# Kernel optimization log

Hardware: AMD Instinct MI355X
Metric: run time of the kernel (lower is better)

Reference implementation:

```python
import jax, jax.numpy as jnp
import numpy as np

B, S, D = 2, 2048, 2048
H, HD = 16, 128
ROPE_BASE = 10000.0


def _rope(x):
    # x: [B, H, S, HD]; standard rotate-half RoPE with base 10000
    half = x.shape[-1] // 2
    inv_freq = 1.0 / (ROPE_BASE ** (jnp.arange(half, dtype=jnp.float32) / half))
    pos = jnp.arange(x.shape[2], dtype=jnp.float32)
    freqs = pos[:, None] * inv_freq[None, :]           # [S, half]
    cos = jnp.concatenate([jnp.cos(freqs), jnp.cos(freqs)], axis=-1)  # [S, HD]
    sin = jnp.concatenate([jnp.sin(freqs), jnp.sin(freqs)], axis=-1)
    x_rot = jnp.concatenate([-x[..., half:], x[..., :half]], axis=-1)
    return x * cos[None, None, :, :] + x_rot * sin[None, None, :, :]


def setup_inputs() -> dict:
    key = jax.random.key(0)
    kx, kq, ko = jax.random.split(key, 3)
    x = jax.random.normal(kx, (B, S, D), dtype=jnp.float32)
    # weights stored [in, out] (transposed torch Linear weight), no bias
    W_qkv = jax.random.normal(kq, (D, 3 * H * HD), dtype=jnp.float32) * (D ** -0.5)
    W_o = jax.random.normal(ko, (H * HD, D), dtype=jnp.float32) * ((H * HD) ** -0.5)
    return {"x": x, "W_qkv": W_qkv, "W_o": W_o}


def reference(x, W_qkv, W_o):
    b, s, _ = x.shape
    qkv = x @ W_qkv                                    # [B, S, 3*H*HD]
    q, k, v = jnp.split(qkv, 3, axis=-1)
    def heads(t):
        return t.reshape(b, s, H, HD).transpose(0, 2, 1, 3)  # [B, H, S, HD]
    q, k, v = heads(q), heads(k), heads(v)
    q = _rope(q)
    k = _rope(k)
    scores = jnp.einsum("bhqd,bhkd->bhqk", q, k) * (HD ** -0.5)
    causal = jnp.tril(jnp.ones((s, s), dtype=bool))
    scores = jnp.where(causal[None, None, :, :], scores, jnp.float32(-jnp.inf))
    attn = jax.nn.softmax(scores, axis=-1)
    out = jnp.einsum("bhqk,bhkd->bhqd", attn, v)       # [B, H, S, HD]
    out = out.transpose(0, 2, 1, 3).reshape(b, s, H * HD)
    return out @ W_o
```

## Files before the change

kernel.cpp:

```cpp
#include <hip/hip_runtime.h>
#include <math.h>


#define B_    2
#define S_    2048
#define D_    2048
#define H_    16
#define HD_   128
#define M_    (B_ * S_)
#define NQKV_ (3 * H_ * HD_)

typedef __bf16 bf16x8 __attribute__((ext_vector_type(8)));
typedef float  f32x4  __attribute__((ext_vector_type(4)));
typedef unsigned short u16x8 __attribute__((ext_vector_type(8)));

__device__ __forceinline__ unsigned short f32_bf16(float f) {
  unsigned int u = __float_as_uint(f);
  u = (u + 0x7fffu + ((u >> 16) & 1u)) >> 16;
  return (unsigned short)u;
}
__device__ __forceinline__ float bf16_f32(unsigned short u) {
  return __uint_as_float(((unsigned int)u) << 16);
}

__device__ __forceinline__ void gload_lds16(const void* g, void* lds) {
  __builtin_amdgcn_global_load_lds(
      (const __attribute__((address_space(1))) unsigned int*)g,
      (__attribute__((address_space(3))) unsigned int*)lds, 16, 0, 0);
}

__global__ __launch_bounds__(256) void cvt_bf16_kernel(
    const float* __restrict__ in, unsigned short* __restrict__ out, int n4) {
  int i = blockIdx.x * blockDim.x + threadIdx.x;
  if (i >= n4) return;
  float4 v = ((const float4*)in)[i];
  ((ushort4*)out)[i] =
      make_ushort4(f32_bf16(v.x), f32_bf16(v.y), f32_bf16(v.z), f32_bf16(v.w));
}

__global__ __launch_bounds__(1024) void cvt_t_kernel(
    const float* __restrict__ in, unsigned short* __restrict__ out,
    int K, int ldin, int ncol0) {
  __shared__ float t[32][33];
  const int n0 = blockIdx.x * 32, k0 = blockIdx.y * 32;
  const int tx = threadIdx.x & 31, ty = threadIdx.x >> 5;
  t[ty][tx] = in[(size_t)(k0 + ty) * ldin + ncol0 + n0 + tx];
  __syncthreads();
  out[(size_t)(n0 + ty) * K + k0 + tx] = f32_bf16(t[tx][ty]);
}

__global__ __launch_bounds__(256) void rope_bf16_kernel(
    unsigned short* __restrict__ qkv) {
  const int row = blockIdx.x;
  const int sec = blockIdx.y * 4 + (threadIdx.x >> 6);
  const int d   = threadIdx.x & 63;
  const int pos = row & (S_ - 1);
  float invf = exp2f(-(float)d * (13.287712379549449f / 64.0f));
  float ang = (float)pos * invf;
  float sn, cs;
  sincosf(ang, &sn, &cs);
  unsigned short* p = qkv + (size_t)row * NQKV_ + sec * HD_ + d;
  float x1 = bf16_f32(p[0]), x2 = bf16_f32(p[64]);
  p[0]  = f32_bf16(x1 * cs - x2 * sn);
  p[64] = f32_bf16(x2 * cs + x1 * sn);
}

template <bool OUT_BF16>
__global__ __launch_bounds__(256) void gemm_bt_bf16(
    const unsigned short* __restrict__ A, const unsigned short* __restrict__ Bt,
    void* __restrict__ Cv, int M, int N, int K, int ldc) {
  constexpr int BK = 32;
  __shared__ __align__(16) unsigned short As[128 * BK];
  __shared__ __align__(16) unsigned short Bs[128 * BK];
  const int tid = threadIdx.x;
  const int wid = tid >> 6, lane = tid & 63;
  const int wr = wid >> 1, wc = wid & 1;
  const int m0 = blockIdx.y * 128, n0 = blockIdx.x * 128;

  const char* Ab = (const char*)(A + (size_t)m0 * K);
  const char* Bb = (const char*)(Bt + (size_t)n0 * K);
  char* AsB = (char*)As;
  char* BsB = (char*)Bs;
  const size_t rowbytes = (size_t)K * 2;

  f32x4 acc[4][4];
#pragma unroll
  for (int i = 0; i < 4; ++i)
#pragma unroll
    for (int j = 0; j < 4; ++j) acc[i][j] = (f32x4){0.f, 0.f, 0.f, 0.f};

  const int r16 = lane & 15, kg = lane >> 4;

  for (int k0 = 0; k0 < K; k0 += BK) {
#pragma unroll
    for (int c = 0; c < 2; ++c) {
      int q = wid * 128 + c * 64 + lane;
      size_t goff = (size_t)(q >> 2) * rowbytes + (size_t)k0 * 2 + (q & 3) * 16;
      int loff = wid * 2048 + c * 1024;
      gload_lds16(Ab + goff, AsB + loff);
      gload_lds16(Bb + goff, BsB + loff);
    }
    __syncthreads();

    bf16x8 af[4], bfr[4];
#pragma unroll
    for (int i = 0; i < 4; ++i)
      af[i] = *(const bf16x8*)(As + (wr * 64 + i * 16 + r16) * BK + kg * 8);
#pragma unroll
    for (int j = 0; j < 4; ++j)
      bfr[j] = *(const bf16x8*)(Bs + (wc * 64 + j * 16 + r16) * BK + kg * 8);
#pragma unroll
    for (int i = 0; i < 4; ++i)
#pragma unroll
      for (int j = 0; j < 4; ++j)
        acc[i][j] = __builtin_amdgcn_mfma_f32_16x16x32_bf16(af[i], bfr[j],
                                                            acc[i][j], 0, 0, 0);
    __syncthreads();
  }

#pragma unroll
  for (int i = 0; i < 4; ++i) {
    int row = m0 + wr * 64 + i * 16 + (lane >> 4) * 4;
#pragma unroll
    for (int j = 0; j < 4; ++j) {
      int col = n0 + wc * 64 + j * 16 + (lane & 15);
      if constexpr (OUT_BF16) {
        unsigned short* cp = (unsigned short*)Cv + (size_t)row * ldc + col;
        cp[0]               = f32_bf16(acc[i][j][0]);
        cp[(size_t)ldc]     = f32_bf16(acc[i][j][1]);
        cp[(size_t)2 * ldc] = f32_bf16(acc[i][j][2]);
        cp[(size_t)3 * ldc] = f32_bf16(acc[i][j][3]);
      } else {
        float* cp = (float*)Cv + (size_t)row * ldc + col;
        cp[0]               = acc[i][j][0];
        cp[(size_t)ldc]     = acc[i][j][1];
        cp[(size_t)2 * ldc] = acc[i][j][2];
        cp[(size_t)3 * ldc] = acc[i][j][3];
      }
    }
  }
}

__global__ __launch_bounds__(256) void attn_mfma_kernel(
    const unsigned short* __restrict__ qkv, unsigned short* __restrict__ out) {
  const int qt = (int)gridDim.x - 1 - (int)blockIdx.x;
  const int bh = blockIdx.y;
  const int b = bh >> 4, h = bh & (H_ - 1);
  const int tid = threadIdx.x;
  const int w = tid >> 6, lane = tid & 63;
  const int r16 = lane & 15, kg = lane >> 4;

  __shared__ __align__(16) unsigned short Qs[64 * 128];
  __shared__ __align__(16) unsigned short Ks[64 * 128];
  __shared__ __align__(16) unsigned short Vt[128 * 72];
  __shared__ __align__(16) unsigned short Ps[4][16 * 72];

  const unsigned short* Qg = qkv + ((size_t)b * S_ + (size_t)qt * 64) * NQKV_ + h * HD_;
  const unsigned short* Kg = qkv + (size_t)b * S_ * NQKV_ + H_ * HD_ + h * HD_;
  const unsigned short* Vg = qkv + (size_t)b * S_ * NQKV_ + 2 * H_ * HD_ + h * HD_;

#pragma unroll
  for (int it = 0; it < 4; ++it) {
    int q = w * 256 + it * 64 + lane;
    int row = q >> 4, c = q & 15;
    int gc = c ^ (row & 7);
    gload_lds16(Qg + (size_t)row * NQKV_ + gc * 8, (char*)Qs + q * 16);
  }

  float m_i[4], l_i[4];
  f32x4 accO[8];
#pragma unroll
  for (int r = 0; r < 4; ++r) { m_i[r] = -INFINITY; l_i[r] = 0.f; }
#pragma unroll
  for (int jd = 0; jd < 8; ++jd) accO[jd] = (f32x4){0.f, 0.f, 0.f, 0.f};

  const float scale = 0.08838834764831845f;
  const int qg_row = qt * 64 + w * 16 + kg * 4;
  const int nkt = qt + 1;

  for (int kt = 0; kt < nkt; ++kt) {
    const int kv0 = kt * 64;
    __syncthreads();

#pragma unroll
    for (int it = 0; it < 4; ++it) {
      int q = w * 256 + it * 64 + lane;
      int row = q >> 4, c = q & 15;
      int gc = c ^ (row & 7);
      gload_lds16(Kg + (size_t)(kv0 + row) * NQKV_ + gc * 8, (char*)Ks + q * 16);
    }
    {
      const unsigned short* vr = Vg + (size_t)(kv0 + lane) * NQKV_;
#pragma unroll
      for (int it = 0; it < 4; ++it) {
        int dc = w + it * 4;
        u16x8 v = *(const u16x8*)(vr + dc * 8);
#pragma unroll
        for (int j = 0; j < 8; ++j) Vt[(dc * 8 + j) * 72 + lane] = v[j];
      }
    }
    __syncthreads();

    f32x4 sc[4];
#pragma unroll
    for (int j = 0; j < 4; ++j) sc[j] = (f32x4){0.f, 0.f, 0.f, 0.f};
    {
      const int arow = w * 16 + r16;
      bf16x8 aq[4];
#pragma unroll
      for (int ks = 0; ks < 4; ++ks)
        aq[ks] = *(const bf16x8*)((const char*)Qs + arow * 256 +
                                  (((ks * 4 + kg) ^ (arow & 7)) * 16));
#pragma unroll
      for (int ks = 0; ks < 4; ++ks) {
#pragma unroll
        for (int j = 0; j < 4; ++j) {
          const int brow = j * 16 + r16;
          bf16x8 bk = *(const bf16x8*)((const char*)Ks + brow * 256 +
                                       (((ks * 4 + kg) ^ (brow & 7)) * 16));
          sc[j] = __builtin_amdgcn_mfma_f32_16x16x32_bf16(aq[ks], bk, sc[j], 0, 0, 0);
        }
      }
    }

    const bool diag = (kt == qt);
    float alpha[4];
#pragma unroll
    for (int r = 0; r < 4; ++r) {
      float sv[4];
#pragma unroll
      for (int j = 0; j < 4; ++j) {
        sv[j] = sc[j][r] * scale;
        if (diag && (kv0 + j * 16 + r16 > qg_row + r)) sv[j] = -INFINITY;
      }
      float tmax = fmaxf(fmaxf(sv[0], sv[1]), fmaxf(sv[2], sv[3]));
#pragma unroll
      for (int off = 8; off > 0; off >>= 1)
        tmax = fmaxf(tmax, __shfl_xor(tmax, off, 16));
      float mn = fmaxf(m_i[r], tmax);
      alpha[r] = __expf(m_i[r] - mn);
      m_i[r] = mn;
      float rs = 0.f;
#pragma unroll
      for (int j = 0; j < 4; ++j) {
        float p = __expf(sv[j] - mn);
        rs += p;
        Ps[w][(kg * 4 + r) * 72 + j * 16 + r16] = f32_bf16(p);
      }
#pragma unroll
      for (int off = 8; off > 0; off >>= 1) rs += __shfl_xor(rs, off, 16);
      l_i[r] = l_i[r] * alpha[r] + rs;
    }

#pragma unroll
    for (int jd = 0; jd < 8; ++jd)
#pragma unroll
      for (int r = 0; r < 4; ++r) accO[jd][r] *= alpha[r];

#pragma unroll
    for (int ks2 = 0; ks2 < 2; ++ks2) {
      bf16x8 pf = *(const bf16x8*)((const char*)&Ps[w][0] + r16 * 144 +
                                   ks2 * 64 + kg * 16);
#pragma unroll
      for (int jd = 0; jd < 8; ++jd) {
        bf16x8 vf = *(const bf16x8*)((const char*)Vt + (jd * 16 + r16) * 144 +
                                     ks2 * 64 + kg * 16);
        accO[jd] = __builtin_amdgcn_mfma_f32_16x16x32_bf16(pf, vf, accO[jd], 0, 0, 0);
      }
    }
  }

  unsigned short* ob = out + ((size_t)b * S_ + (size_t)qt * 64 + w * 16) * (H_ * HD_) +
                       h * HD_;
#pragma unroll
  for (int r = 0; r < 4; ++r) {
    float inv_l = 1.0f / l_i[r];
    unsigned short* orow = ob + (size_t)(kg * 4 + r) * (H_ * HD_);
#pragma unroll
    for (int jd = 0; jd < 8; ++jd)
      orow[jd * 16 + r16] = f32_bf16(accO[jd][r] * inv_l);
  }
}

extern "C" void kernel_launch(void* const* d_in, const int* in_sizes, int n_in,
                              void* d_out, int out_size, void* d_ws, size_t ws_size,
                              hipStream_t stream) {
  const float* x    = (const float*)d_in[0];
  const float* Wqkv = (const float*)d_in[1];
  const float* Wo   = (const float*)d_in[2];
  float* out = (float*)d_out;

  char* ws = (char*)d_ws;
  unsigned short* qkvb  = (unsigned short*)ws;
  unsigned short* xb    = (unsigned short*)(ws + 50331648);
  unsigned short* attnb = xb;
  unsigned short* wt    = (unsigned short*)(ws + 67108864);

  cvt_bf16_kernel<<<(M_ * D_ / 4 + 255) / 256, 256, 0, stream>>>(x, xb, M_ * D_ / 4);

  for (int s = 0; s < 3; ++s) {
    cvt_t_kernel<<<dim3(D_ / 32, D_ / 32), 1024, 0, stream>>>(
        Wqkv, wt, D_, NQKV_, s * D_);
    gemm_bt_bf16<true><<<dim3(D_ / 128, M_ / 128), 256, 0, stream>>>(
        xb, wt, qkvb + (size_t)s * D_, M_, D_, D_, NQKV_);
  }

  rope_bf16_kernel<<<dim3(M_, 8), 256, 0, stream>>>(qkvb);

  attn_mfma_kernel<<<dim3(S_ / 64, B_ * H_), 256, 0, stream>>>(qkvb, attnb);

  cvt_t_kernel<<<dim3(D_ / 32, D_ / 32), 1024, 0, stream>>>(Wo, wt, H_ * HD_, D_, 0);
  gemm_bt_bf16<false><<<dim3(D_ / 128, M_ / 128), 256, 0, stream>>>(
      attnb, wt, out, M_, D_, H_ * HD_, D_);
}
```

Baseline: 625.3 us.

## Widen attention query tile to 128 with Q in registers; fuse QKV GEMM launches

```diff
diff --git a/kernel.cpp b/kernel.cpp
--- a/kernel.cpp
+++ b/kernel.cpp
@@ -141,7 +141,7 @@
   }
 }
 
-__global__ __launch_bounds__(256) void attn_mfma_kernel(
+__global__ __launch_bounds__(512, 4) void attn_mfma_kernel(
     const unsigned short* __restrict__ qkv, unsigned short* __restrict__ out) {
   const int qt = (int)gridDim.x - 1 - (int)blockIdx.x;
   const int bh = blockIdx.y;
@@ -150,22 +150,19 @@
   const int w = tid >> 6, lane = tid & 63;
   const int r16 = lane & 15, kg = lane >> 4;
 
-  __shared__ __align__(16) unsigned short Qs[64 * 128];
   __shared__ __align__(16) unsigned short Ks[64 * 128];
   __shared__ __align__(16) unsigned short Vt[128 * 72];
-  __shared__ __align__(16) unsigned short Ps[4][16 * 72];
-
-  const unsigned short* Qg = qkv + ((size_t)b * S_ + (size_t)qt * 64) * NQKV_ + h * HD_;
+  __shared__ __align__(16) unsigned short Ps[8][16 * 72];
+
   const unsigned short* Kg = qkv + (size_t)b * S_ * NQKV_ + H_ * HD_ + h * HD_;
   const unsigned short* Vg = qkv + (size_t)b * S_ * NQKV_ + 2 * H_ * HD_ + h * HD_;
 
-#pragma unroll
-  for (int it = 0; it < 4; ++it) {
-    int q = w * 256 + it * 64 + lane;
-    int row = q >> 4, c = q & 15;
-    int gc = c ^ (row & 7);
-    gload_lds16(Qg + (size_t)row * NQKV_ + gc * 8, (char*)Qs + q * 16);
-  }
+  const unsigned short* Qg =
+      qkv + ((size_t)b * S_ + (size_t)qt * 128 + w * 16 + r16) * NQKV_ + h * HD_;
+  bf16x8 aq[4];
+#pragma unroll
+  for (int ks = 0; ks < 4; ++ks)
+    aq[ks] = *(const bf16x8*)(Qg + ks * 32 + kg * 8);
 
   float m_i[4], l_i[4];
   f32x4 accO[8];
@@ -175,16 +172,17 @@
   for (int jd = 0; jd < 8; ++jd) accO[jd] = (f32x4){0.f, 0.f, 0.f, 0.f};
 
   const float scale = 0.08838834764831845f;
-  const int qg_row = qt * 64 + w * 16 + kg * 4;
-  const int nkt = qt + 1;
+  const int qg_row = qt * 128 + w * 16 + kg * 4;
+  const int wave_qmin = qt * 128 + w * 16;
+  const int nkt = 2 * (qt + 1);
 
   for (int kt = 0; kt < nkt; ++kt) {
     const int kv0 = kt * 64;
     __syncthreads();
 
 #pragma unroll
-    for (int it = 0; it < 4; ++it) {
-      int q = w * 256 + it * 64 + lane;
+    for (int it = 0; it < 2; ++it) {
+      int q = (w * 2 + it) * 64 + lane;
       int row = q >> 4, c = q & 15;
       int gc = c ^ (row & 7);
       gload_lds16(Kg + (size_t)(kv0 + row) * NQKV_ + gc * 8, (char*)Ks + q * 16);
@@ -192,8 +190,8 @@
     {
       const unsigned short* vr = Vg + (size_t)(kv0 + lane) * NQKV_;
 #pragma unroll
-      for (int it = 0; it < 4; ++it) {
-        int dc = w + it * 4;
+      for (int it = 0; it < 2; ++it) {
+        int dc = w + it * 8;
         u16x8 v = *(const u16x8*)(vr + dc * 8);
 #pragma unroll
         for (int j = 0; j < 8; ++j) Vt[(dc * 8 + j) * 72 + lane] = v[j];
@@ -204,26 +202,18 @@
     f32x4 sc[4];
 #pragma unroll
     for (int j = 0; j < 4; ++j) sc[j] = (f32x4){0.f, 0.f, 0.f, 0.f};
-    {
-      const int arow = w * 16 + r16;
-      bf16x8 aq[4];
-#pragma unroll
-      for (int ks = 0; ks < 4; ++ks)
-        aq[ks] = *(const bf16x8*)((const char*)Qs + arow * 256 +
-                                  (((ks * 4 + kg) ^ (arow & 7)) * 16));
-#pragma unroll
-      for (int ks = 0; ks < 4; ++ks) {
-#pragma unroll
-        for (int j = 0; j < 4; ++j) {
-          const int brow = j * 16 + r16;
-          bf16x8 bk = *(const bf16x8*)((const char*)Ks + brow * 256 +
-                                       (((ks * 4 + kg) ^ (brow & 7)) * 16));
-          sc[j] = __builtin_amdgcn_mfma_f32_16x16x32_bf16(aq[ks], bk, sc[j], 0, 0, 0);
-        }
-      }
-    }
-
-    const bool diag = (kt == qt);
+#pragma unroll
+    for (int ks = 0; ks < 4; ++ks) {
+#pragma unroll
+      for (int j = 0; j < 4; ++j) {
+        const int brow = j * 16 + r16;
+        bf16x8 bk = *(const bf16x8*)((const char*)Ks + brow * 256 +
+                                     (((ks * 4 + kg) ^ (brow & 7)) * 16));
+        sc[j] = __builtin_amdgcn_mfma_f32_16x16x32_bf16(aq[ks], bk, sc[j], 0, 0, 0);
+      }
+    }
+
+    const bool diag = (kv0 + 63 > wave_qmin);
     float alpha[4];
 #pragma unroll
     for (int r = 0; r < 4; ++r) {
@@ -270,8 +260,8 @@
     }
   }
 
-  unsigned short* ob = out + ((size_t)b * S_ + (size_t)qt * 64 + w * 16) * (H_ * HD_) +
-                       h * HD_;
+  unsigned short* ob = out +
+      ((size_t)b * S_ + (size_t)qt * 128 + w * 16) * (H_ * HD_) + h * HD_;
 #pragma unroll
   for (int r = 0; r < 4; ++r) {
     float inv_l = 1.0f / l_i[r];
@@ -298,16 +288,14 @@
 
   cvt_bf16_kernel<<<(M_ * D_ / 4 + 255) / 256, 256, 0, stream>>>(x, xb, M_ * D_ / 4);
 
-  for (int s = 0; s < 3; ++s) {
-    cvt_t_kernel<<<dim3(D_ / 32, D_ / 32), 1024, 0, stream>>>(
-        Wqkv, wt, D_, NQKV_, s * D_);
-    gemm_bt_bf16<true><<<dim3(D_ / 128, M_ / 128), 256, 0, stream>>>(
-        xb, wt, qkvb + (size_t)s * D_, M_, D_, D_, NQKV_);
-  }
+  cvt_t_kernel<<<dim3(NQKV_ / 32, D_ / 32), 1024, 0, stream>>>(
+      Wqkv, wt, D_, NQKV_, 0);
+  gemm_bt_bf16<true><<<dim3(NQKV_ / 128, M_ / 128), 256, 0, stream>>>(
+      xb, wt, qkvb, M_, NQKV_, D_, NQKV_);
 
   rope_bf16_kernel<<<dim3(M_, 8), 256, 0, stream>>>(qkvb);
 
-  attn_mfma_kernel<<<dim3(S_ / 64, B_ * H_), 256, 0, stream>>>(qkvb, attnb);
+  attn_mfma_kernel<<<dim3(S_ / 128, B_ * H_), 512, 0, stream>>>(qkvb, attnb);
 
   cvt_t_kernel<<<dim3(D_ / 32, D_ / 32), 1024, 0, stream>>>(Wo, wt, H_ * HD_, D_, 0);
   gemm_bt_bf16<false><<<dim3(D_ / 128, M_ / 128), 256, 0, stream>>>(
```

After: 506.8 us. 1.23x faster.
